# Kernel tuning notes

Measured on AMD Instinct MI355X. Metric: run time of the kernel, lower is better.

The kernel has to match this reference:

```python
import jax, jax.numpy as jnp
import numpy as np

B, D, T = 8, 512, 2048
K = 8192


def setup_inputs() -> dict:
    key = jax.random.key(0)
    k1, k2 = jax.random.split(key)
    latents = jax.random.normal(k1, (B, D, T), dtype=jnp.float32)
    # nn.Embedding weight init: uniform(-1/K, 1/K)
    embedding = jax.random.uniform(k2, (K, D), dtype=jnp.float32,
                                   minval=-1.0 / K, maxval=1.0 / K)
    return {"latents": latents, "embedding": embedding}


def reference(latents, embedding):
    # latents: [B, D, T] -> [B, T, D]
    x = jnp.transpose(latents, (0, 2, 1))
    # squared Euclidean distances (argmin identical to cdist p=2 argmin)
    x2 = jnp.sum(x * x, axis=-1, keepdims=True)          # [B, T, 1]
    e2 = jnp.sum(embedding * embedding, axis=-1)          # [K]
    xe = jnp.einsum('btd,kd->btk', x, embedding)          # [B, T, K]
    d2 = x2 - 2.0 * xe + e2                               # [B, T, K]
    ids = jnp.argmin(d2, axis=-1)                         # [B, T] int
    quantized = embedding[ids]                            # [B, T, D] gather
    return jnp.transpose(quantized, (0, 2, 1))            # [B, D, T]
```

## Files before the change

kernel.cpp:

```cpp
#include <hip/hip_runtime.h>

#define B 8
#define D 512
#define T 2048
#define K 8192
#define M (B*T)

typedef float f32x4 __attribute__((ext_vector_type(4)));
typedef short bf16x8 __attribute__((ext_vector_type(8)));
typedef unsigned short us8 __attribute__((ext_vector_type(8)));

#define CAP_SEG 48
#define WIN 1.6e-3f

#define WS_X2    0
#define WS_E2    65536
#define WS_CNT   98304
#define WS_IDS   163840
#define WS_OVFC  229376
#define WS_OVFL  229632
#define WS_BEST  295168
#define WS_GMIN  426240
#define WS_LIST  491776
#define WS_AX    6783232
#define WS_BE    23560448
#define WS_NEED  31949056

__device__ inline unsigned short f2bf(float f) {
    unsigned int x = __float_as_uint(f);
    unsigned int r = x + 0x7fffu + ((x >> 16) & 1u);
    return (unsigned short)(r >> 16);
}

__device__ inline unsigned int f2ord(float f) {
    unsigned int u = __float_as_uint(f);
    return (u & 0x80000000u) ? ~u : (u | 0x80000000u);
}
__device__ inline float ord2f(unsigned int u) {
    return __uint_as_float((u & 0x80000000u) ? (u & 0x7fffffffu) : ~u);
}

__device__ inline void gload16(const void* g, void* l) {
    __builtin_amdgcn_global_load_lds(
        (const __attribute__((address_space(1))) unsigned int*)g,
        (__attribute__((address_space(3))) unsigned int*)l, 16, 0, 0);
}

__global__ __launch_bounds__(256)
void vq_init(unsigned int* __restrict__ cnt_seg_u32, int* __restrict__ ovfc,
             unsigned int* __restrict__ gmin) {
    int i = blockIdx.x * 256 + threadIdx.x;
    cnt_seg_u32[i] = 0;
    gmin[i] = 0xFFFFFFFFu;
    if (i == 0) *ovfc = 0;
}

__global__ __launch_bounds__(256)
void vq_x2_kernel(const float* __restrict__ lat, float* __restrict__ x2g) {
#pragma clang fp contract(off)
    int p = blockIdx.x * 256 + threadIdx.x;
    int b = p / T, t = p % T;
    const float* base = lat + (size_t)b * D * T + t;
    float blk[4];
#pragma unroll
    for (int q = 0; q < 4; q++) {
        float r[8];
#pragma unroll
        for (int j = 0; j < 8; j++) {
            float v = base[(size_t)(q * 128 + j) * T];
            r[j] = __fmul_rn(v, v);
        }
        for (int i = 8; i < 128; i += 8) {
#pragma unroll
            for (int j = 0; j < 8; j++) {
                float v = base[(size_t)(q * 128 + i + j) * T];
                r[j] = __fadd_rn(r[j], __fmul_rn(v, v));
            }
        }
        blk[q] = __fadd_rn(__fadd_rn(__fadd_rn(r[0], r[1]), __fadd_rn(r[2], r[3])),
                           __fadd_rn(__fadd_rn(r[4], r[5]), __fadd_rn(r[6], r[7])));
    }
    x2g[p] = __fadd_rn(__fadd_rn(blk[0], blk[1]), __fadd_rn(blk[2], blk[3]));
}

__global__ __launch_bounds__(256)
void vq_e2_kernel(const float* __restrict__ emb, float* __restrict__ e2g) {
#pragma clang fp contract(off)
    int k = blockIdx.x * 256 + threadIdx.x;
    const float* base = emb + (size_t)k * D;
    float blk[4];
#pragma unroll
    for (int q = 0; q < 4; q++) {
        float r[8];
        {
            float4 a = *(const float4*)&base[q * 128];
            float4 c = *(const float4*)&base[q * 128 + 4];
            r[0] = __fmul_rn(a.x, a.x); r[1] = __fmul_rn(a.y, a.y);
            r[2] = __fmul_rn(a.z, a.z); r[3] = __fmul_rn(a.w, a.w);
            r[4] = __fmul_rn(c.x, c.x); r[5] = __fmul_rn(c.y, c.y);
            r[6] = __fmul_rn(c.z, c.z); r[7] = __fmul_rn(c.w, c.w);
        }
        for (int i = 8; i < 128; i += 8) {
            float4 a = *(const float4*)&base[q * 128 + i];
            float4 c = *(const float4*)&base[q * 128 + i + 4];
            r[0] = __fadd_rn(r[0], __fmul_rn(a.x, a.x));
            r[1] = __fadd_rn(r[1], __fmul_rn(a.y, a.y));
            r[2] = __fadd_rn(r[2], __fmul_rn(a.z, a.z));
            r[3] = __fadd_rn(r[3], __fmul_rn(a.w, a.w));
            r[4] = __fadd_rn(r[4], __fmul_rn(c.x, c.x));
            r[5] = __fadd_rn(r[5], __fmul_rn(c.y, c.y));
            r[6] = __fadd_rn(r[6], __fmul_rn(c.z, c.z));
            r[7] = __fadd_rn(r[7], __fmul_rn(c.w, c.w));
        }
        blk[q] = __fadd_rn(__fadd_rn(__fadd_rn(r[0], r[1]), __fadd_rn(r[2], r[3])),
                           __fadd_rn(__fadd_rn(r[4], r[5]), __fadd_rn(r[6], r[7])));
    }
    e2g[k] = __fadd_rn(__fadd_rn(blk[0], blk[1]), __fadd_rn(blk[2], blk[3]));
}

__global__ __launch_bounds__(256)
void vq_prep_a(const float* __restrict__ lat, unsigned short* __restrict__ Ax) {
    __shared__ float xsl[64][65];
    const int tid = threadIdx.x;
    const int m0 = blockIdx.x * 64;
    const int b = m0 / T, t0 = m0 % T;
    const float* lp = lat + (size_t)b * D * T + t0;
    for (int d0 = 0; d0 < D; d0 += 64) {
        if (d0) __syncthreads();
#pragma unroll
        for (int i = 0; i < 16; i++) {
            int idx = tid + i * 256;
            int dd = idx >> 6, tt = idx & 63;
            xsl[dd][tt] = lp[(size_t)(d0 + dd) * T + tt];
        }
        __syncthreads();
        int tt = tid & 63, g = tid >> 6;
        us8 va, vb;
#pragma unroll
        for (int j = 0; j < 8; j++) va[j] = f2bf(xsl[g * 16 + j][tt]);
#pragma unroll
        for (int j = 0; j < 8; j++) vb[j] = f2bf(xsl[g * 16 + 8 + j][tt]);
        *(us8*)&Ax[(size_t)(m0 + tt) * 512 + d0 + g * 16] = va;
        *(us8*)&Ax[(size_t)(m0 + tt) * 512 + d0 + g * 16 + 8] = vb;
    }
}

__global__ __launch_bounds__(256)
void vq_prep_b(const float* __restrict__ emb, unsigned short* __restrict__ Be) {
    size_t i = ((size_t)blockIdx.x * 256 + threadIdx.x) * 4;
    float4 v = *(const float4*)&emb[i];
    ushort4 o;
    o.x = f2bf(v.x); o.y = f2bf(v.y); o.z = f2bf(v.z); o.w = f2bf(v.w);
    *(ushort4*)&Be[i] = o;
}

#define BMg 128
#define BNg 128
#define NCHUNK 2048
#define NSTEPS ((NCHUNK / BNg) * 8)

__global__ __launch_bounds__(256, 2)
void vq_gemm(const unsigned short* __restrict__ Ax,
             const unsigned short* __restrict__ Be,
             const float* __restrict__ e2g,
             unsigned int* __restrict__ gmin,
             unsigned char* __restrict__ cnt_seg,
             unsigned short* __restrict__ list) {
    __shared__ unsigned short As[2][BMg * 64];
    __shared__ unsigned short Bs[2][BNg * 64];
    __shared__ float e2s[NCHUNK];
    __shared__ int cntl[BMg];

    const int tid = threadIdx.x;
    const int lane = tid & 63;
    const int wid = tid >> 6;
    const int m0 = blockIdx.x * BMg;
    const int nc0 = blockIdx.y * NCHUNK;

    for (int i = tid; i < NCHUNK; i += 256) e2s[i] = e2g[nc0 + i];
    if (tid < BMg) cntl[tid] = 0;
    asm volatile("s_waitcnt lgkmcnt(0)" ::: "memory");

    const int rbase = wid * 8 + (lane >> 3);
    const int cbyte = (((lane & 7) ^ (lane >> 3)) * 16);
    const char* gA = (const char*)Ax + (size_t)(m0 + rbase) * 1024 + cbyte;
    const char* gB = (const char*)Be + (size_t)(nc0 + rbase) * 1024 + cbyte;
    const int ldsoff = wid * 1024;

    const int rbyteA = (wid * 32 + (lane & 15)) * 128;
    const int rbyteB = ((lane & 15)) * 128;

#pragma unroll
    for (int i = 0; i < 4; i++) {
        gload16(gA + (size_t)i * 32768, (char*)As[0] + ldsoff + i * 4096);
        gload16(gB + (size_t)i * 32768, (char*)Bs[0] + ldsoff + i * 4096);
    }

    float runmin[2][4];
    float thrg[2][4];
#pragma unroll
    for (int mi = 0; mi < 2; mi++)
#pragma unroll
        for (int r = 0; r < 4; r++) runmin[mi][r] = 3.4e38f;

    f32x4 acc[2][8];
    for (int s = 0; s < NSTEPS; s++) {
        const int cur = s & 1;
        const int nt = s >> 3, ks = s & 7;

        __builtin_amdgcn_s_barrier();

        if (s + 1 < NSTEPS) {
            const int nt2 = (s + 1) >> 3, ks2 = (s + 1) & 7;
            const char* ga = gA + (size_t)(ks2 * 128);
            const char* gb = gB + (size_t)(nt2 * 128) * 1024 + (size_t)(ks2 * 128);
            char* la = (char*)As[cur ^ 1] + ldsoff;
            char* lb = (char*)Bs[cur ^ 1] + ldsoff;
#pragma unroll
            for (int i = 0; i < 4; i++) {
                gload16(ga + (size_t)i * 32768, la + i * 4096);
                gload16(gb + (size_t)i * 32768, lb + i * 4096);
            }
            asm volatile("s_waitcnt vmcnt(8)" ::: "memory");
        } else {
            asm volatile("s_waitcnt vmcnt(0)" ::: "memory");
        }
        __builtin_amdgcn_s_barrier();

        if (ks == 0) {
#pragma unroll
            for (int mi = 0; mi < 2; mi++)
#pragma unroll
                for (int ni = 0; ni < 8; ni++) acc[mi][ni] = (f32x4){0.f, 0.f, 0.f, 0.f};
#pragma unroll
            for (int mi = 0; mi < 2; mi++)
#pragma unroll
                for (int r = 0; r < 4; r++) {
                    const int m = m0 + wid * 32 + mi * 16 + (lane >> 4) * 4 + r;
                    thrg[mi][r] = ord2f(gmin[m]);
                }
        }

        __builtin_amdgcn_s_setprio(1);
#pragma unroll
        for (int kh = 0; kh < 2; kh++) {
            const int cb = ((((lane >> 4) + kh * 4) ^ (lane & 7)) * 16);
            bf16x8 af[2], bfr[8];
#pragma unroll
            for (int mi = 0; mi < 2; mi++)
                af[mi] = *(const bf16x8*)((const char*)As[cur] + rbyteA + mi * 2048 + cb);
#pragma unroll
            for (int ni = 0; ni < 8; ni++)
                bfr[ni] = *(const bf16x8*)((const char*)Bs[cur] + rbyteB + ni * 2048 + cb);
#pragma unroll
            for (int mi = 0; mi < 2; mi++)
#pragma unroll
                for (int ni = 0; ni < 8; ni++)
                    acc[mi][ni] = __builtin_amdgcn_mfma_f32_16x16x32_bf16(
                        af[mi], bfr[ni], acc[mi][ni], 0, 0, 0);
        }
        __builtin_amdgcn_s_setprio(0);

        if (ks == 7) {
            const int n0l = nt * BNg;
#pragma unroll
            for (int mi = 0; mi < 2; mi++)
#pragma unroll
                for (int ni = 0; ni < 8; ni++) {
                    float e2v = e2s[n0l + ni * 16 + (lane & 15)];
#pragma unroll
                    for (int r = 0; r < 4; r++)
                        acc[mi][ni][r] = e2v - 2.0f * acc[mi][ni][r];
                }
#pragma unroll
            for (int mi = 0; mi < 2; mi++)
#pragma unroll
                for (int r = 0; r < 4; r++) {
                    float v = acc[mi][0][r];
#pragma unroll
                    for (int ni = 1; ni < 8; ni++) v = fminf(v, acc[mi][ni][r]);
                    v = fminf(v, __shfl_xor(v, 1));
                    v = fminf(v, __shfl_xor(v, 2));
                    v = fminf(v, __shfl_xor(v, 4));
                    v = fminf(v, __shfl_xor(v, 8));
                    runmin[mi][r] = fminf(runmin[mi][r], v);
                    const int rloc = wid * 32 + mi * 16 + (lane >> 4) * 4 + r;
                    const int m = m0 + rloc;
                    float th = fminf(thrg[mi][r], runmin[mi][r]) + WIN;
#pragma unroll
                    for (int ni = 0; ni < 8; ni++) {
                        if (acc[mi][ni][r] < th) {
                            int kcode = nc0 + n0l + ni * 16 + (lane & 15);
                            int slot = atomicAdd(&cntl[rloc], 1);
                            if (slot < CAP_SEG)
                                list[m * 192 + blockIdx.y * CAP_SEG + slot] =
                                    (unsigned short)kcode;
                        }
                    }
                    if ((lane & 15) == 0)
                        atomicMin(&gmin[m], f2ord(runmin[mi][r]));
                }
        }
    }

    __syncthreads();
    if (tid < BMg) {
        int c = cntl[tid];
        cnt_seg[(size_t)(m0 + tid) * 4 + blockIdx.y] =
            (unsigned char)(c > 255 ? 255 : c);
    }
}

__global__ __launch_bounds__(256)
void vq_rescore3(const float* __restrict__ lat, const float* __restrict__ emb,
                 const float* __restrict__ x2g, const float* __restrict__ e2g,
                 const unsigned char* __restrict__ cnt_seg,
                 const unsigned short* __restrict__ list,
                 int* __restrict__ ids, int* __restrict__ ovfc,
                 int* __restrict__ ovfl, unsigned long long* __restrict__ best) {
#pragma clang fp contract(off)
    __shared__ float xs[D][32];
    __shared__ unsigned long long bests[8][32];
    __shared__ int ovfs[32];

    const int tid = threadIdx.x;
    const int w = tid >> 5;
    const int l = tid & 31;
    const int m0 = blockIdx.x * 32;
    const int b = m0 / T, t0 = m0 % T;
    const int p = m0 + l;
    const size_t lbase = (size_t)b * D * T + t0;

#pragma unroll
    for (int i = 0; i < 64; i++) {
        int idx = tid + i * 256;
        int dd = idx >> 5, tt = idx & 31;
        xs[dd][tt] = lat[lbase + (size_t)dd * T + tt];
    }

    unsigned int cs = *(const unsigned int*)&cnt_seg[(size_t)p * 4];
    int c0 = cs & 255, c1 = (cs >> 8) & 255, c2 = (cs >> 16) & 255, c3 = (cs >> 24) & 255;
    const bool ovf = (c0 > CAP_SEG) | (c1 > CAP_SEG) | (c2 > CAP_SEG) | (c3 > CAP_SEG);
    if (w == 0) {
        ovfs[l] = ovf;
        if (ovf) {
            int s = atomicAdd(ovfc, 1);
            ovfl[s] = p;
            best[p] = ~0ull;
        }
    }
    __syncthreads();

    const float x2v = x2g[p];
    unsigned long long bb = ~0ull;
    if (!ovf) {
        int segc[4] = {c0, c1, c2, c3};
#pragma unroll
        for (int seg = 0; seg < 4; seg++) {
            for (int j = w; j < segc[seg]; j += 8) {
                int k = list[(size_t)p * 192 + seg * CAP_SEG + j];
                const float4* er4 = (const float4*)(emb + (size_t)k * D);
                float acc = 0.f;
#pragma unroll 4
                for (int q = 0; q < D / 4; q++) {
                    float4 e4 = er4[q];
                    acc = __fadd_rn(acc, __fmul_rn(xs[q * 4 + 0][l], e4.x));
                    acc = __fadd_rn(acc, __fmul_rn(xs[q * 4 + 1][l], e4.y));
                    acc = __fadd_rn(acc, __fmul_rn(xs[q * 4 + 2][l], e4.z));
                    acc = __fadd_rn(acc, __fmul_rn(xs[q * 4 + 3][l], e4.w));
                }
                float tmp = __fsub_rn(x2v, __fadd_rn(acc, acc));
                float dist = __fadd_rn(tmp, e2g[k]);
                unsigned long long pk = ((unsigned long long)f2ord(dist) << 32) |
                                        (unsigned long long)(unsigned int)k;
                bb = (pk < bb) ? pk : bb;
            }
        }
    }
    bests[w][l] = bb;
    __syncthreads();

    if (tid < 32 && !ovfs[tid]) {
        unsigned long long v = bests[0][tid];
#pragma unroll
        for (int i = 1; i < 8; i++) v = (bests[i][tid] < v) ? bests[i][tid] : v;
        ids[m0 + tid] = (int)(v & 0xFFFFFFFFull);
    }
}

__global__ __launch_bounds__(256)
void vq_fallback_par(const float* __restrict__ lat, const float* __restrict__ emb,
                     const float* __restrict__ x2g, const float* __restrict__ e2g,
                     const int* __restrict__ ovfc, const int* __restrict__ ovfl,
                     unsigned long long* __restrict__ best) {
#pragma clang fp contract(off)
    __shared__ float xr[D];
    __shared__ unsigned long long wmin[4];
    const int n = *ovfc;
    const int ntask = n * 8;
    for (int task = blockIdx.x; task < ntask; task += gridDim.x) {
        const int m = ovfl[task >> 3];
        const int slice = task & 7;
        const int b = m / T, t = m % T;
        for (int d = threadIdx.x; d < D; d += 256)
            xr[d] = lat[(size_t)b * D * T + (size_t)d * T + t];
        __syncthreads();
        const float x2v = x2g[m];
        unsigned long long bl = ~0ull;
        for (int k = slice * 1024 + threadIdx.x; k < slice * 1024 + 1024; k += 256) {
            const float* er = emb + (size_t)k * D;
            float s = 0.f;
            for (int d = 0; d < D; d++)
                s = __fadd_rn(s, __fmul_rn(xr[d], er[d]));
            float tmp = __fsub_rn(x2v, __fadd_rn(s, s));
            float dist = __fadd_rn(tmp, e2g[k]);
            unsigned long long pk = ((unsigned long long)f2ord(dist) << 32) |
                                    (unsigned long long)(unsigned int)k;
            bl = (pk < bl) ? pk : bl;
        }
#pragma unroll
        for (int off = 1; off < 64; off <<= 1) {
            unsigned long long o = __shfl_xor(bl, off);
            bl = (o < bl) ? o : bl;
        }
        if ((threadIdx.x & 63) == 0) wmin[threadIdx.x >> 6] = bl;
        __syncthreads();
        if (threadIdx.x == 0) {
            unsigned long long v = wmin[0];
            for (int i = 1; i < 4; i++) v = (wmin[i] < v) ? wmin[i] : v;
            atomicMin(&best[m], v);
        }
        __syncthreads();
    }
}

__global__ __launch_bounds__(256)
void vq_finalize(const int* __restrict__ ovfc, const int* __restrict__ ovfl,
                 const unsigned long long* __restrict__ best, int* __restrict__ ids) {
    const int n = *ovfc;
    for (int i = blockIdx.x * 256 + threadIdx.x; i < n; i += gridDim.x * 256) {
        int m = ovfl[i];
        ids[m] = (int)(best[m] & 0xFFFFFFFFull);
    }
}

__global__ __launch_bounds__(256)
void vq_gather(const float* __restrict__ emb, const int* __restrict__ ids,
               float* __restrict__ out) {
    __shared__ float gbuf[64][65];
    __shared__ int ids_s[64];
    const int tid = threadIdx.x;
    const int m0 = blockIdx.x * 64;
    const int b = m0 / T, t0 = m0 % T;
    if (tid < 64) ids_s[tid] = ids[m0 + tid];
    float* outb = out + (size_t)b * D * T + t0;
    for (int d0 = 0; d0 < D; d0 += 64) {
        __syncthreads();
#pragma unroll
        for (int i = 0; i < 16; i++) {
            int idx = tid + i * 256;
            int tt = idx >> 6, dd = idx & 63;
            gbuf[tt][dd] = emb[(size_t)ids_s[tt] * D + d0 + dd];
        }
        __syncthreads();
#pragma unroll
        for (int i = 0; i < 16; i++) {
            int idx = tid + i * 256;
            int dd = idx >> 6, tt = idx & 63;
            outb[(size_t)(d0 + dd) * T + tt] = gbuf[tt][dd];
        }
    }
}

#define TM 64
#define TN 128
#define TD 32
__global__ __launch_bounds__(256)
void vq_main_old(const float* __restrict__ latents, const float* __restrict__ emb,
                 const float* __restrict__ x2g, const float* __restrict__ e2g,
                 float* __restrict__ out) {
#pragma clang fp contract(off)
    __shared__ __align__(16) float xs[TD][TM];
    __shared__ __align__(16) float es[TD][TN + 4];
    __shared__ float e2s[TN];
    __shared__ float x2s[TM];
    __shared__ int ids_s[TM];
    __shared__ __align__(16) float gbuf[64][65];
    const int tid = threadIdx.x;
    const int tn = tid & 15;
    const int tm = tid >> 4;
    const int m0 = blockIdx.x * TM;
    const int b = m0 / T;
    const int t0 = m0 % T;
    const float* lat = latents + (size_t)b * D * T + t0;
    if (tid < TM) x2s[tid] = x2g[m0 + tid];
    float minv[4];
    int mini[4];
#pragma unroll
    for (int i = 0; i < 4; i++) { minv[i] = 3.4e38f; mini[i] = 0; }
    for (int k0 = 0; k0 < K; k0 += TN) {
        __syncthreads();
        if (tid < TN) e2s[tid] = e2g[k0 + tid];
        float s[4][8];
#pragma unroll
        for (int i = 0; i < 4; i++)
#pragma unroll
            for (int j = 0; j < 8; j++) s[i][j] = 0.0f;
        for (int d0 = 0; d0 < D; d0 += TD) {
            if (d0) __syncthreads();
#pragma unroll
            for (int i = 0; i < 8; i++) {
                int idx = tid + i * 256;
                int dd = idx >> 6, tt = idx & 63;
                xs[dd][tt] = lat[(size_t)(d0 + dd) * T + tt];
            }
#pragma unroll
            for (int i = 0; i < 16; i++) {
                int idx = tid + i * 256;
                int nn = idx >> 5, dd = idx & 31;
                es[dd][nn] = emb[(size_t)(k0 + nn) * D + d0 + dd];
            }
            __syncthreads();
#pragma unroll
            for (int d = 0; d < TD; d++) {
                float4 xr = *(const float4*)&xs[d][tm * 4];
                float4 ea = *(const float4*)&es[d][tn * 4];
                float4 eb = *(const float4*)&es[d][64 + tn * 4];
                float xv[4] = {xr.x, xr.y, xr.z, xr.w};
                float ev[8] = {ea.x, ea.y, ea.z, ea.w, eb.x, eb.y, eb.z, eb.w};
#pragma unroll
                for (int i = 0; i < 4; i++)
#pragma unroll
                    for (int j = 0; j < 8; j++)
                        s[i][j] = __fadd_rn(s[i][j], __fmul_rn(xv[i], ev[j]));
            }
        }
#pragma unroll
        for (int i = 0; i < 4; i++) {
            float x2v = x2s[tm * 4 + i];
#pragma unroll
            for (int j = 0; j < 8; j++) {
                int col = (j < 4) ? (tn * 4 + j) : (64 + tn * 4 + (j - 4));
                float s2 = __fadd_rn(s[i][j], s[i][j]);
                float tmp = __fsub_rn(x2v, s2);
                float dist = __fadd_rn(tmp, e2s[col]);
                int kk = k0 + col;
                if (dist < minv[i]) { minv[i] = dist; mini[i] = kk; }
            }
        }
    }
#pragma unroll
    for (int i = 0; i < 4; i++) {
        float v1 = minv[i];
        int i1 = mini[i];
#pragma unroll
        for (int off = 1; off < 16; off <<= 1) {
            float ov = __shfl_xor(v1, off);
            int oi = __shfl_xor(i1, off);
            if (ov < v1 || (ov == v1 && oi < i1)) { v1 = ov; i1 = oi; }
        }
        if (tn == 0) ids_s[tm * 4 + i] = i1;
    }
    __syncthreads();
    float* outb = out + (size_t)b * D * T + t0;
    for (int d0 = 0; d0 < D; d0 += 64) {
        if (d0) __syncthreads();
#pragma unroll
        for (int i = 0; i < 16; i++) {
            int idx = tid + i * 256;
            int tt = idx >> 6, dd = idx & 63;
            gbuf[tt][dd] = emb[(size_t)ids_s[tt] * D + d0 + dd];
        }
        __syncthreads();
#pragma unroll
        for (int i = 0; i < 16; i++) {
            int idx = tid + i * 256;
            int dd = idx >> 6, tt = idx & 63;
            outb[(size_t)(d0 + dd) * T + tt] = gbuf[tt][dd];
        }
    }
}

extern "C" void kernel_launch(void* const* d_in, const int* in_sizes, int n_in,
                              void* d_out, int out_size, void* d_ws, size_t ws_size,
                              hipStream_t stream) {
    const float* latents = (const float*)d_in[0];
    const float* emb     = (const float*)d_in[1];
    float* out = (float*)d_out;
    char* ws = (char*)d_ws;
    float* x2g = (float*)(ws + WS_X2);
    float* e2g = (float*)(ws + WS_E2);

    if (ws_size < (size_t)WS_NEED) {
        hipLaunchKernelGGL(vq_x2_kernel, dim3(M / 256), dim3(256), 0, stream, latents, x2g);
        hipLaunchKernelGGL(vq_e2_kernel, dim3(K / 256), dim3(256), 0, stream, emb, e2g);
        hipLaunchKernelGGL(vq_main_old, dim3(M / TM), dim3(256), 0, stream,
                           latents, emb, x2g, e2g, out);
        return;
    }

    unsigned char* cnt_seg = (unsigned char*)(ws + WS_CNT);
    int* ids = (int*)(ws + WS_IDS);
    int* ovfc = (int*)(ws + WS_OVFC);
    int* ovfl = (int*)(ws + WS_OVFL);
    unsigned long long* best = (unsigned long long*)(ws + WS_BEST);
    unsigned int* gmin = (unsigned int*)(ws + WS_GMIN);
    unsigned short* list = (unsigned short*)(ws + WS_LIST);
    unsigned short* Ax = (unsigned short*)(ws + WS_AX);
    unsigned short* Be = (unsigned short*)(ws + WS_BE);

    hipLaunchKernelGGL(vq_init, dim3(M / 256), dim3(256), 0, stream,
                       (unsigned int*)cnt_seg, ovfc, gmin);
    hipLaunchKernelGGL(vq_x2_kernel, dim3(M / 256), dim3(256), 0, stream, latents, x2g);
    hipLaunchKernelGGL(vq_e2_kernel, dim3(K / 256), dim3(256), 0, stream, emb, e2g);
    hipLaunchKernelGGL(vq_prep_a, dim3(M / 64), dim3(256), 0, stream, latents, Ax);
    hipLaunchKernelGGL(vq_prep_b, dim3((K * D) / 1024), dim3(256), 0, stream, emb, Be);
    hipLaunchKernelGGL(vq_gemm, dim3(M / BMg, K / NCHUNK), dim3(256), 0, stream,
                       Ax, Be, e2g, gmin, cnt_seg, list);
    hipLaunchKernelGGL(vq_rescore3, dim3(M / 32), dim3(256), 0, stream,
                       latents, emb, x2g, e2g, cnt_seg, list, ids, ovfc, ovfl, best);
    hipLaunchKernelGGL(vq_fallback_par, dim3(2048), dim3(256), 0, stream,
                       latents, emb, x2g, e2g, ovfc, ovfl, best);
    hipLaunchKernelGGL(vq_finalize, dim3(64), dim3(256), 0, stream,
                       ovfc, ovfl, best, ids);
    hipLaunchKernelGGL(vq_gather, dim3(M / 64), dim3(256), 0, stream, emb, ids, out);
}
```

Before: 483.0 us.

## Enlarge GEMM block tile to 256x256 with 8 waves in 2x4 layout

Doubles the vq_gemm block tile to 256 rows by 256 codes and uses 512 threads arranged as a 2x4 wave grid, each wave computing a 128x64 sub-tile. The goal is more data reuse per LDS load and fewer global loads of A and B. The per-row global minimum threshold moves into shared memory, and a __syncthreads is added in the epilogue. LDS use roughly doubles and accumulator register pressure rises, which may cut occupancy. The fallback kernel grid also shrinks.

```diff
diff --git a/kernel.cpp b/kernel.cpp
--- a/kernel.cpp
+++ b/kernel.cpp
@@ -154,12 +154,12 @@
     *(ushort4*)&Be[i] = o;
 }
 
-#define BMg 128
-#define BNg 128
+#define BMg 256
+#define BNg 256
 #define NCHUNK 2048
 #define NSTEPS ((NCHUNK / BNg) * 8)
 
-__global__ __launch_bounds__(256, 2)
+__global__ __launch_bounds__(512, 2)
 void vq_gemm(const unsigned short* __restrict__ Ax,
              const unsigned short* __restrict__ Be,
              const float* __restrict__ e2g,
@@ -169,41 +169,45 @@
     __shared__ unsigned short As[2][BMg * 64];
     __shared__ unsigned short Bs[2][BNg * 64];
     __shared__ float e2s[NCHUNK];
+    __shared__ float gminl[BMg];
     __shared__ int cntl[BMg];
 
     const int tid = threadIdx.x;
     const int lane = tid & 63;
     const int wid = tid >> 6;
+    const int wr = wid >> 2;
+    const int wc = wid & 3;
     const int m0 = blockIdx.x * BMg;
     const int nc0 = blockIdx.y * NCHUNK;
 
-    for (int i = tid; i < NCHUNK; i += 256) e2s[i] = e2g[nc0 + i];
+    for (int i = tid; i < NCHUNK; i += 512) e2s[i] = e2g[nc0 + i];
     if (tid < BMg) cntl[tid] = 0;
     asm volatile("s_waitcnt lgkmcnt(0)" ::: "memory");
 
     const int rbase = wid * 8 + (lane >> 3);
     const int cbyte = (((lane & 7) ^ (lane >> 3)) * 16);
     const char* gA = (const char*)Ax + (size_t)(m0 + rbase) * 1024 + cbyte;
-    const char* gB = (const char*)Be + (size_t)(nc0 + rbase) * 1024 + cbyte;
+    const char* gB0 = (const char*)Be + (size_t)(nc0 + rbase) * 1024 + cbyte;
     const int ldsoff = wid * 1024;
 
-    const int rbyteA = (wid * 32 + (lane & 15)) * 128;
-    const int rbyteB = ((lane & 15)) * 128;
+    const int rbyteA = (wr * 128 + (lane & 15)) * 128;
+    const int rbyteB = (wc * 64 + (lane & 15)) * 128;
 
 #pragma unroll
     for (int i = 0; i < 4; i++) {
-        gload16(gA + (size_t)i * 32768, (char*)As[0] + ldsoff + i * 4096);
-        gload16(gB + (size_t)i * 32768, (char*)Bs[0] + ldsoff + i * 4096);
-    }
-
-    float runmin[2][4];
-    float thrg[2][4];
-#pragma unroll
-    for (int mi = 0; mi < 2; mi++)
+        gload16(gA + (size_t)i * 65536, (char*)As[0] + ldsoff + i * 8192);
+        gload16(gB0 + (size_t)i * 65536, (char*)Bs[0] + ldsoff + i * 8192);
+    }
+
+    float runmin[8][4];
+#pragma unroll
+    for (int mi = 0; mi < 8; mi++)
 #pragma unroll
         for (int r = 0; r < 4; r++) runmin[mi][r] = 3.4e38f;
 
-    f32x4 acc[2][8];
+    float vth = 3.4e38f;
+    f32x4 acc[8][4];
+
     for (int s = 0; s < NSTEPS; s++) {
         const int cur = s & 1;
         const int nt = s >> 3, ks = s & 7;
@@ -213,13 +217,13 @@
         if (s + 1 < NSTEPS) {
             const int nt2 = (s + 1) >> 3, ks2 = (s + 1) & 7;
             const char* ga = gA + (size_t)(ks2 * 128);
-            const char* gb = gB + (size_t)(nt2 * 128) * 1024 + (size_t)(ks2 * 128);
+            const char* gb = gB0 + (size_t)(nt2 * 256) * 1024 + (size_t)(ks2 * 128);
             char* la = (char*)As[cur ^ 1] + ldsoff;
             char* lb = (char*)Bs[cur ^ 1] + ldsoff;
 #pragma unroll
             for (int i = 0; i < 4; i++) {
-                gload16(ga + (size_t)i * 32768, la + i * 4096);
-                gload16(gb + (size_t)i * 32768, lb + i * 4096);
+                gload16(ga + (size_t)i * 65536, la + i * 8192);
+                gload16(gb + (size_t)i * 65536, lb + i * 8192);
             }
             asm volatile("s_waitcnt vmcnt(8)" ::: "memory");
         } else {
@@ -229,68 +233,63 @@
 
         if (ks == 0) {
 #pragma unroll
-            for (int mi = 0; mi < 2; mi++)
-#pragma unroll
-                for (int ni = 0; ni < 8; ni++) acc[mi][ni] = (f32x4){0.f, 0.f, 0.f, 0.f};
-#pragma unroll
-            for (int mi = 0; mi < 2; mi++)
-#pragma unroll
-                for (int r = 0; r < 4; r++) {
-                    const int m = m0 + wid * 32 + mi * 16 + (lane >> 4) * 4 + r;
-                    thrg[mi][r] = ord2f(gmin[m]);
-                }
+            for (int mi = 0; mi < 8; mi++)
+#pragma unroll
+                for (int ni = 0; ni < 4; ni++) acc[mi][ni] = (f32x4){0.f, 0.f, 0.f, 0.f};
+            if (tid < BMg) vth = ord2f(gmin[m0 + tid]);
         }
 
         __builtin_amdgcn_s_setprio(1);
 #pragma unroll
-        for (int kh = 0; kh < 2; kh++) {
-            const int cb = ((((lane >> 4) + kh * 4) ^ (lane & 7)) * 16);
-            bf16x8 af[2], bfr[8];
-#pragma unroll
-            for (int mi = 0; mi < 2; mi++)
-                af[mi] = *(const bf16x8*)((const char*)As[cur] + rbyteA + mi * 2048 + cb);
-#pragma unroll
-            for (int ni = 0; ni < 8; ni++)
+        for (int kk = 0; kk < 2; kk++) {
+            const int cb = ((((lane >> 4) + kk * 4) ^ (lane & 7)) * 16);
+            bf16x8 bfr[4];
+#pragma unroll
+            for (int ni = 0; ni < 4; ni++)
                 bfr[ni] = *(const bf16x8*)((const char*)Bs[cur] + rbyteB + ni * 2048 + cb);
 #pragma unroll
-            for (int mi = 0; mi < 2; mi++)
-#pragma unroll
-                for (int ni = 0; ni < 8; ni++)
+            for (int mi = 0; mi < 8; mi++) {
+                bf16x8 af = *(const bf16x8*)((const char*)As[cur] + rbyteA + mi * 2048 + cb);
+#pragma unroll
+                for (int ni = 0; ni < 4; ni++)
                     acc[mi][ni] = __builtin_amdgcn_mfma_f32_16x16x32_bf16(
-                        af[mi], bfr[ni], acc[mi][ni], 0, 0, 0);
+                        af, bfr[ni], acc[mi][ni], 0, 0, 0);
+            }
         }
         __builtin_amdgcn_s_setprio(0);
 
         if (ks == 7) {
             const int n0l = nt * BNg;
-#pragma unroll
-            for (int mi = 0; mi < 2; mi++)
-#pragma unroll
-                for (int ni = 0; ni < 8; ni++) {
-                    float e2v = e2s[n0l + ni * 16 + (lane & 15)];
+            if (tid < BMg) gminl[tid] = vth;
+            __syncthreads();
+#pragma unroll
+            for (int mi = 0; mi < 8; mi++)
+#pragma unroll
+                for (int ni = 0; ni < 4; ni++) {
+                    float e2v = e2s[n0l + wc * 64 + ni * 16 + (lane & 15)];
 #pragma unroll
                     for (int r = 0; r < 4; r++)
                         acc[mi][ni][r] = e2v - 2.0f * acc[mi][ni][r];
                 }
 #pragma unroll
-            for (int mi = 0; mi < 2; mi++)
+            for (int mi = 0; mi < 8; mi++)
 #pragma unroll
                 for (int r = 0; r < 4; r++) {
                     float v = acc[mi][0][r];
 #pragma unroll
-                    for (int ni = 1; ni < 8; ni++) v = fminf(v, acc[mi][ni][r]);
+                    for (int ni = 1; ni < 4; ni++) v = fminf(v, acc[mi][ni][r]);
                     v = fminf(v, __shfl_xor(v, 1));
                     v = fminf(v, __shfl_xor(v, 2));
                     v = fminf(v, __shfl_xor(v, 4));
                     v = fminf(v, __shfl_xor(v, 8));
                     runmin[mi][r] = fminf(runmin[mi][r], v);
-                    const int rloc = wid * 32 + mi * 16 + (lane >> 4) * 4 + r;
+                    const int rloc = wr * 128 + mi * 16 + (lane >> 4) * 4 + r;
                     const int m = m0 + rloc;
-                    float th = fminf(thrg[mi][r], runmin[mi][r]) + WIN;
-#pragma unroll
-                    for (int ni = 0; ni < 8; ni++) {
+                    float th = fminf(gminl[rloc], runmin[mi][r]) + WIN;
+#pragma unroll
+                    for (int ni = 0; ni < 4; ni++) {
                         if (acc[mi][ni][r] < th) {
-                            int kcode = nc0 + n0l + ni * 16 + (lane & 15);
+                            int kcode = nc0 + n0l + wc * 64 + ni * 16 + (lane & 15);
                             int slot = atomicAdd(&cntl[rloc], 1);
                             if (slot < CAP_SEG)
                                 list[m * 192 + blockIdx.y * CAP_SEG + slot] =
@@ -615,11 +614,11 @@
     hipLaunchKernelGGL(vq_e2_kernel, dim3(K / 256), dim3(256), 0, stream, emb, e2g);
     hipLaunchKernelGGL(vq_prep_a, dim3(M / 64), dim3(256), 0, stream, latents, Ax);
     hipLaunchKernelGGL(vq_prep_b, dim3((K * D) / 1024), dim3(256), 0, stream, emb, Be);
-    hipLaunchKernelGGL(vq_gemm, dim3(M / BMg, K / NCHUNK), dim3(256), 0, stream,
+    hipLaunchKernelGGL(vq_gemm, dim3(M / BMg, K / NCHUNK), dim3(512), 0, stream,
                        Ax, Be, e2g, gmin, cnt_seg, list);
     hipLaunchKernelGGL(vq_rescore3, dim3(M / 32), dim3(256), 0, stream,
                        latents, emb, x2g, e2g, cnt_seg, list, ids, ovfc, ovfl, best);
-    hipLaunchKernelGGL(vq_fallback_par, dim3(2048), dim3(256), 0, stream,
+    hipLaunchKernelGGL(vq_fallback_par, dim3(512), dim3(256), 0, stream,
                        latents, emb, x2g, e2g, ovfc, ovfl, best);
     hipLaunchKernelGGL(vq_finalize, dim3(64), dim3(256), 0, stream,
                        ovfc, ovfl, best, ids);
```

Result: slower. 591.0 us (+22.4%).

## Fuse output gather into rescore and merge x2 with init kernel

Applied to the files above, without the earlier changes.

The rescore kernel now writes quantized output rows directly, reusing its shared xs buffer for the transposing stage. This removes the separate full gather pass. Only overflow rows are gathered afterward by a small kernel. The init kernel is merged with the x2 norm kernel to save one launch, and the fallback grid shrinks from 2048 to 512 blocks. The risk is extra shared-memory staging and syncs inside rescore, plus an uncoalesced per-row gather for overflow rows.

```diff
diff --git a/kernel.cpp b/kernel.cpp
--- a/kernel.cpp
+++ b/kernel.cpp
@@ -47,12 +47,36 @@
 }
 
 __global__ __launch_bounds__(256)
-void vq_init(unsigned int* __restrict__ cnt_seg_u32, int* __restrict__ ovfc,
-             unsigned int* __restrict__ gmin) {
-    int i = blockIdx.x * 256 + threadIdx.x;
-    cnt_seg_u32[i] = 0;
-    gmin[i] = 0xFFFFFFFFu;
-    if (i == 0) *ovfc = 0;
+void vq_x2_init(const float* __restrict__ lat, float* __restrict__ x2g,
+                unsigned int* __restrict__ cnt_seg_u32, int* __restrict__ ovfc,
+                unsigned int* __restrict__ gmin) {
+#pragma clang fp contract(off)
+    int p = blockIdx.x * 256 + threadIdx.x;
+    cnt_seg_u32[p] = 0;
+    gmin[p] = 0xFFFFFFFFu;
+    if (p == 0) *ovfc = 0;
+    int b = p / T, t = p % T;
+    const float* base = lat + (size_t)b * D * T + t;
+    float blk[4];
+#pragma unroll
+    for (int q = 0; q < 4; q++) {
+        float r[8];
+#pragma unroll
+        for (int j = 0; j < 8; j++) {
+            float v = base[(size_t)(q * 128 + j) * T];
+            r[j] = __fmul_rn(v, v);
+        }
+        for (int i = 8; i < 128; i += 8) {
+#pragma unroll
+            for (int j = 0; j < 8; j++) {
+                float v = base[(size_t)(q * 128 + i + j) * T];
+                r[j] = __fadd_rn(r[j], __fmul_rn(v, v));
+            }
+        }
+        blk[q] = __fadd_rn(__fadd_rn(__fadd_rn(r[0], r[1]), __fadd_rn(r[2], r[3])),
+                           __fadd_rn(__fadd_rn(r[4], r[5]), __fadd_rn(r[6], r[7])));
+    }
+    x2g[p] = __fadd_rn(__fadd_rn(blk[0], blk[1]), __fadd_rn(blk[2], blk[3]));
 }
 
 __global__ __launch_bounds__(256)
@@ -317,11 +341,12 @@
                  const unsigned char* __restrict__ cnt_seg,
                  const unsigned short* __restrict__ list,
                  int* __restrict__ ids, int* __restrict__ ovfc,
-                 int* __restrict__ ovfl, unsigned long long* __restrict__ best) {
+                 int* __restrict__ ovfl, unsigned long long* __restrict__ best,
+                 float* __restrict__ out) {
 #pragma clang fp contract(off)
     __shared__ float xs[D][32];
     __shared__ unsigned long long bests[8][32];
-    __shared__ int ovfs[32];
+    __shared__ int kid_s[32];
 
     const int tid = threadIdx.x;
     const int w = tid >> 5;
@@ -341,13 +366,10 @@
     unsigned int cs = *(const unsigned int*)&cnt_seg[(size_t)p * 4];
     int c0 = cs & 255, c1 = (cs >> 8) & 255, c2 = (cs >> 16) & 255, c3 = (cs >> 24) & 255;
     const bool ovf = (c0 > CAP_SEG) | (c1 > CAP_SEG) | (c2 > CAP_SEG) | (c3 > CAP_SEG);
-    if (w == 0) {
-        ovfs[l] = ovf;
-        if (ovf) {
-            int s = atomicAdd(ovfc, 1);
-            ovfl[s] = p;
-            best[p] = ~0ull;
-        }
+    if (w == 0 && ovf) {
+        int s = atomicAdd(ovfc, 1);
+        ovfl[s] = p;
+        best[p] = ~0ull;
     }
     __syncthreads();
 
@@ -380,11 +402,42 @@
     bests[w][l] = bb;
     __syncthreads();
 
-    if (tid < 32 && !ovfs[tid]) {
-        unsigned long long v = bests[0][tid];
-#pragma unroll
-        for (int i = 1; i < 8; i++) v = (bests[i][tid] < v) ? bests[i][tid] : v;
-        ids[m0 + tid] = (int)(v & 0xFFFFFFFFull);
+    if (tid < 32) {
+        unsigned int cs2 = *(const unsigned int*)&cnt_seg[(size_t)(m0 + tid) * 4];
+        bool ov2 = ((cs2 & 255) > CAP_SEG) | (((cs2 >> 8) & 255) > CAP_SEG) |
+                   (((cs2 >> 16) & 255) > CAP_SEG) | (((cs2 >> 24) & 255) > CAP_SEG);
+        if (!ov2) {
+            unsigned long long v = bests[0][tid];
+#pragma unroll
+            for (int i = 1; i < 8; i++) v = (bests[i][tid] < v) ? bests[i][tid] : v;
+            int kk = (int)(v & 0xFFFFFFFFull);
+            ids[m0 + tid] = kk;
+            kid_s[tid] = kk;
+        } else {
+            kid_s[tid] = -1;
+        }
+    }
+    __syncthreads();
+
+    float* ebuf = &xs[0][0];
+    float* outb = out + (size_t)b * D * T + t0;
+    for (int d0 = 0; d0 < D; d0 += 64) {
+        if (d0) __syncthreads();
+#pragma unroll
+        for (int i = 0; i < 8; i++) {
+            int idx = tid + i * 256;
+            int tt = idx >> 6, dd = idx & 63;
+            int kk = kid_s[tt];
+            ebuf[tt * 65 + dd] = emb[(size_t)(kk < 0 ? 0 : kk) * D + d0 + dd];
+        }
+        __syncthreads();
+#pragma unroll
+        for (int i = 0; i < 8; i++) {
+            int idx = tid + i * 256;
+            int tt = idx & 31, dd = idx >> 5;
+            if (kid_s[tt] >= 0)
+                outb[(size_t)(d0 + dd) * T + tt] = ebuf[tt * 65 + dd];
+        }
     }
 }
 
@@ -445,30 +498,16 @@
 }
 
 __global__ __launch_bounds__(256)
-void vq_gather(const float* __restrict__ emb, const int* __restrict__ ids,
-               float* __restrict__ out) {
-    __shared__ float gbuf[64][65];
-    __shared__ int ids_s[64];
-    const int tid = threadIdx.x;
-    const int m0 = blockIdx.x * 64;
-    const int b = m0 / T, t0 = m0 % T;
-    if (tid < 64) ids_s[tid] = ids[m0 + tid];
-    float* outb = out + (size_t)b * D * T + t0;
-    for (int d0 = 0; d0 < D; d0 += 64) {
-        __syncthreads();
-#pragma unroll
-        for (int i = 0; i < 16; i++) {
-            int idx = tid + i * 256;
-            int tt = idx >> 6, dd = idx & 63;
-            gbuf[tt][dd] = emb[(size_t)ids_s[tt] * D + d0 + dd];
-        }
-        __syncthreads();
-#pragma unroll
-        for (int i = 0; i < 16; i++) {
-            int idx = tid + i * 256;
-            int dd = idx >> 6, tt = idx & 63;
-            outb[(size_t)(d0 + dd) * T + tt] = gbuf[tt][dd];
-        }
+void vq_gather_ovf(const float* __restrict__ emb, const int* __restrict__ ovfc,
+                   const int* __restrict__ ovfl, const int* __restrict__ ids,
+                   float* __restrict__ out) {
+    const int n = *ovfc;
+    for (int i = blockIdx.x; i < n; i += gridDim.x) {
+        int m = ovfl[i];
+        int b = m / T, t = m % T;
+        int k = ids[m];
+        for (int d = threadIdx.x; d < D; d += 256)
+            out[(size_t)b * D * T + (size_t)d * T + t] = emb[(size_t)k * D + d];
     }
 }
 
@@ -609,19 +648,19 @@
     unsigned short* Ax = (unsigned short*)(ws + WS_AX);
     unsigned short* Be = (unsigned short*)(ws + WS_BE);
 
-    hipLaunchKernelGGL(vq_init, dim3(M / 256), dim3(256), 0, stream,
-                       (unsigned int*)cnt_seg, ovfc, gmin);
-    hipLaunchKernelGGL(vq_x2_kernel, dim3(M / 256), dim3(256), 0, stream, latents, x2g);
+    hipLaunchKernelGGL(vq_x2_init, dim3(M / 256), dim3(256), 0, stream,
+                       latents, x2g, (unsigned int*)cnt_seg, ovfc, gmin);
     hipLaunchKernelGGL(vq_e2_kernel, dim3(K / 256), dim3(256), 0, stream, emb, e2g);
     hipLaunchKernelGGL(vq_prep_a, dim3(M / 64), dim3(256), 0, stream, latents, Ax);
     hipLaunchKernelGGL(vq_prep_b, dim3((K * D) / 1024), dim3(256), 0, stream, emb, Be);
     hipLaunchKernelGGL(vq_gemm, dim3(M / BMg, K / NCHUNK), dim3(256), 0, stream,
                        Ax, Be, e2g, gmin, cnt_seg, list);
     hipLaunchKernelGGL(vq_rescore3, dim3(M / 32), dim3(256), 0, stream,
-                       latents, emb, x2g, e2g, cnt_seg, list, ids, ovfc, ovfl, best);
-    hipLaunchKernelGGL(vq_fallback_par, dim3(2048), dim3(256), 0, stream,
+                       latents, emb, x2g, e2g, cnt_seg, list, ids, ovfc, ovfl, best, out);
+    hipLaunchKernelGGL(vq_fallback_par, dim3(512), dim3(256), 0, stream,
                        latents, emb, x2g, e2g, ovfc, ovfl, best);
     hipLaunchKernelGGL(vq_finalize, dim3(64), dim3(256), 0, stream,
                        ovfc, ovfl, best, ids);
-    hipLaunchKernelGGL(vq_gather, dim3(M / 64), dim3(256), 0, stream, emb, ids, out);
-}
+    hipLaunchKernelGGL(vq_gather_ovf, dim3(128), dim3(256), 0, stream,
+                       emb, ovfc, ovfl, ids, out);
+}
```

Measured after the change: 452.7 us. 1.07x faster.
